# Kernel optimization log

Measured on AMD Instinct MI355X. Metric: run time of the kernel, lower is better.

## Reference

```python
import jax, jax.numpy as jnp
import numpy as np
from jax import lax

CROP = 4
DATA_RANGE = 255.0
KSIZE = 11


def _box_filter(x):
    # x: [B,1,H,W]; 11x11 uniform kernel, padding 5 (SAME), single channel
    k = jnp.ones((1, 1, KSIZE, KSIZE), dtype=x.dtype) / (KSIZE * KSIZE)
    return lax.conv_general_dilated(
        x, k, window_strides=(1, 1), padding=[(5, 5), (5, 5)],
        dimension_numbers=("NCHW", "OIHW", "NCHW"))


def setup_inputs() -> dict:
    key = jax.random.key(0)
    k1, k2 = jax.random.split(key)
    img1 = jax.random.uniform(k1, (16, 3, 512, 512), dtype=jnp.float32) * DATA_RANGE
    img2 = jax.random.uniform(k2, (16, 3, 512, 512), dtype=jnp.float32) * DATA_RANGE
    return {"img1": img1, "img2": img2}


def reference(img1, img2):
    # only_test_y_channel: take channel 0
    x1 = img1[:, 0:1, :, :]
    x2 = img2[:, 0:1, :, :]
    # crop_border = 4
    x1 = x1[:, :, CROP:-CROP, CROP:-CROP].astype(jnp.float32)
    x2 = x2[:, :, CROP:-CROP, CROP:-CROP].astype(jnp.float32)

    C1 = (0.01 * DATA_RANGE) ** 2
    C2 = (0.03 * DATA_RANGE) ** 2

    mu1 = _box_filter(x1)
    mu2 = _box_filter(x2)
    mu1_sq = mu1 * mu1
    mu2_sq = mu2 * mu2
    mu1_mu2 = mu1 * mu2
    sigma1_sq = _box_filter(x1 * x1) - mu1_sq
    sigma2_sq = _box_filter(x2 * x2) - mu2_sq
    sigma12 = _box_filter(x1 * x2) - mu1_mu2

    ssim_map = ((2 * mu1_mu2 + C1) * (2 * sigma12 + C2)) / (
        (mu1_sq + mu2_sq + C1) * (sigma1_sq + sigma2_sq + C2))
    return jnp.mean(ssim_map)
```

## Files before the change

### kernel.cpp

```cpp
#include <hip/hip_runtime.h>

#define CROPPX 4
#define H 504
#define W 504
#define IMG 512
#define NB 16
#define NCH 3
#define KS 11
#define RAD 5
#define TW 64
#define STRIP (TW + 2*RAD)
#define RPS 21
#define WPB 4
#define BROWS (RPS * WPB)
#define NYB 6
#define NXT 8
#define TOTAL (RPS + 2*RAD)

__global__ __launch_bounds__(256, 4) void ssim_main(const float* __restrict__ img1,
                                                    const float* __restrict__ img2,
                                                    float* __restrict__ partial) {
    const int lane = threadIdx.x & 63;
    const int wv   = threadIdx.x >> 6;
    const int gx0  = blockIdx.x * TW;
    const int y0   = blockIdx.y * BROWS + wv * RPS;
    const int b    = blockIdx.z;

    __shared__ float2 rowBuf[WPB][STRIP];
    float2* const myRow = rowBuf[wv];

    const float* p1 = img1 + (size_t)(b * NCH) * IMG * IMG + (size_t)CROPPX * IMG + CROPPX;
    const float* p2 = img2 + (size_t)(b * NCH) * IMG * IMG + (size_t)CROPPX * IMG + CROPPX;

    const int  c0   = gx0 - RAD + lane;
    const int  c0c  = min(max(c0, 0), W - 1);
    const bool c0ok = (unsigned)c0 < (unsigned)W;
    const int  c1   = c0 + 64;
    const int  c1c  = min(c1, W - 1);
    const bool c1ok = (unsigned)c1 < (unsigned)W;
    const bool lane2 = lane < (STRIP - 64);

    float r1[KS], r2[KS], r11[KS], r22[KS], r12[KS];
    #pragma unroll
    for (int j = 0; j < KS; ++j) { r1[j]=0.f; r2[j]=0.f; r11[j]=0.f; r22[j]=0.f; r12[j]=0.f; }

    float vs1 = 0.f, vs2 = 0.f, vs11 = 0.f, vs22 = 0.f, vs12 = 0.f;
    float ssum = 0.f;
    const float C1 = 6.5025f, C2 = 58.5225f;
    const float inv121 = 1.0f / 121.0f;
    const bool colValid = (gx0 + lane) < W;

    float a0, b0, a1 = 0.f, b1 = 0.f;
    {
        const int r  = y0 - RAD;
        const int rc = min(max(r, 0), H - 1);
        const bool rok = (unsigned)r < (unsigned)H;
        const size_t ro = (size_t)rc * IMG;
        const float ta0 = p1[ro + c0c], tb0 = p2[ro + c0c];
        a0 = (rok && c0ok) ? ta0 : 0.f;
        b0 = (rok && c0ok) ? tb0 : 0.f;
        if (lane2) {
            const float ta1 = p1[ro + c1c], tb1 = p2[ro + c1c];
            a1 = (rok && c1ok) ? ta1 : 0.f;
            b1 = (rok && c1ok) ? tb1 : 0.f;
        }
    }

    for (int base = 0; base < TOTAL; base += KS) {
        #pragma unroll
        for (int j = 0; j < KS; ++j) {
            const int iter = base + j;
            if (iter >= TOTAL) break;

            myRow[lane] = make_float2(a0, b0);
            if (lane2) myRow[64 + lane] = make_float2(a1, b1);

            if (iter + 1 < TOTAL) {
                const int r  = y0 - RAD + iter + 1;
                const int rc = min(max(r, 0), H - 1);
                const bool rok = (unsigned)r < (unsigned)H;
                const size_t ro = (size_t)rc * IMG;
                const float ta0 = p1[ro + c0c], tb0 = p2[ro + c0c];
                a0 = (rok && c0ok) ? ta0 : 0.f;
                b0 = (rok && c0ok) ? tb0 : 0.f;
                if (lane2) {
                    const float ta1 = p1[ro + c1c], tb1 = p2[ro + c1c];
                    a1 = (rok && c1ok) ? ta1 : 0.f;
                    b1 = (rok && c1ok) ? tb1 : 0.f;
                }
            }

            float h1 = 0.f, h2 = 0.f, h11 = 0.f, h22 = 0.f, h12 = 0.f;
            #pragma unroll
            for (int dx = 0; dx < KS; ++dx) {
                const float2 ab = myRow[lane + dx];
                h1 += ab.x;
                h2 += ab.y;
                h11 = fmaf(ab.x, ab.x, h11);
                h22 = fmaf(ab.y, ab.y, h22);
                h12 = fmaf(ab.x, ab.y, h12);
            }

            vs1  += h1  - r1[j];  r1[j]  = h1;
            vs2  += h2  - r2[j];  r2[j]  = h2;
            vs11 += h11 - r11[j]; r11[j] = h11;
            vs22 += h22 - r22[j]; r22[j] = h22;
            vs12 += h12 - r12[j]; r12[j] = h12;

            if (iter >= 2 * RAD && colValid) {
                const float mu1 = vs1 * inv121;
                const float mu2 = vs2 * inv121;
                const float mu1s = mu1 * mu1;
                const float mu2s = mu2 * mu2;
                const float m12  = mu1 * mu2;
                const float s1  = fmaf(vs11, inv121, -mu1s);
                const float s2  = fmaf(vs22, inv121, -mu2s);
                const float s12 = fmaf(vs12, inv121, -m12);
                const float num = (2.0f * m12 + C1) * (2.0f * s12 + C2);
                const float den = (mu1s + mu2s + C1) * (s1 + s2 + C2);
                ssum = fmaf(num, __builtin_amdgcn_rcpf(den), ssum);
            }
        }
    }

    for (int off = 32; off > 0; off >>= 1)
        ssum += __shfl_down(ssum, off);
    if (lane == 0) {
        const int bidx = (((blockIdx.z * gridDim.y + blockIdx.y) * gridDim.x + blockIdx.x) * WPB) + wv;
        partial[bidx] = ssum;
    }
}

__global__ __launch_bounds__(256) void ssim_final(const float* __restrict__ partial,
                                                  int n, float* __restrict__ out) {
    __shared__ double sh[256];
    double s = 0.0;
    for (int i = threadIdx.x; i < n; i += 256) s += (double)partial[i];
    sh[threadIdx.x] = s;
    __syncthreads();
    for (int stride = 128; stride > 0; stride >>= 1) {
        if (threadIdx.x < stride) sh[threadIdx.x] += sh[threadIdx.x + stride];
        __syncthreads();
    }
    if (threadIdx.x == 0)
        out[0] = (float)(sh[0] / ((double)NB * (double)H * (double)W));
}

extern "C" void kernel_launch(void* const* d_in, const int* in_sizes, int n_in,
                              void* d_out, int out_size, void* d_ws, size_t ws_size,
                              hipStream_t stream) {
    const float* img1 = (const float*)d_in[0];
    const float* img2 = (const float*)d_in[1];
    float* out = (float*)d_out;
    float* partial = (float*)d_ws;

    dim3 grid(NXT, NYB, NB);
    ssim_main<<<grid, 256, 0, stream>>>(img1, img2, partial);
    ssim_final<<<1, 256, 0, stream>>>(partial, NXT * NYB * NB * WPB, out);
}
```

Measured before the change: 145.1 us.

## Replace LDS row staging with per-thread direct global loads of the horizontal window

Removes the shared-memory row buffer. Each thread now loads its own 11-element horizontal window for both images straight from global memory, relying on cache for the overlap between neighbouring lanes. Column out-of-range values are zeroed with a precomputed mask only in edge blocks, and out-of-range rows are zeroed after the horizontal sum. This drops LDS writes and reads, but issues about eleven times more global load instructions per row and needs more registers, so the launch-bounds occupancy hint is lowered from 4 to 3.

```diff
diff --git a/kernel.cpp b/kernel.cpp
--- a/kernel.cpp
+++ b/kernel.cpp
@@ -9,7 +9,6 @@
 #define KS 11
 #define RAD 5
 #define TW 64
-#define STRIP (TW + 2*RAD)
 #define RPS 21
 #define WPB 4
 #define BROWS (RPS * WPB)
@@ -17,7 +16,7 @@
 #define NXT 8
 #define TOTAL (RPS + 2*RAD)
 
-__global__ __launch_bounds__(256, 4) void ssim_main(const float* __restrict__ img1,
+__global__ __launch_bounds__(256, 3) void ssim_main(const float* __restrict__ img1,
                                                     const float* __restrict__ img2,
                                                     float* __restrict__ partial) {
     const int lane = threadIdx.x & 63;
@@ -26,19 +25,18 @@
     const int y0   = blockIdx.y * BROWS + wv * RPS;
     const int b    = blockIdx.z;
 
-    __shared__ float2 rowBuf[WPB][STRIP];
-    float2* const myRow = rowBuf[wv];
-
     const float* p1 = img1 + (size_t)(b * NCH) * IMG * IMG + (size_t)CROPPX * IMG + CROPPX;
     const float* p2 = img2 + (size_t)(b * NCH) * IMG * IMG + (size_t)CROPPX * IMG + CROPPX;
 
-    const int  c0   = gx0 - RAD + lane;
-    const int  c0c  = min(max(c0, 0), W - 1);
-    const bool c0ok = (unsigned)c0 < (unsigned)W;
-    const int  c1   = c0 + 64;
-    const int  c1c  = min(c1, W - 1);
-    const bool c1ok = (unsigned)c1 < (unsigned)W;
-    const bool lane2 = lane < (STRIP - 64);
+    const int  c        = gx0 + lane;
+    const bool colValid = c < W;
+    const int  colBase  = c - RAD;
+    const bool boundary = (blockIdx.x == 0) || (blockIdx.x == NXT - 1);
+
+    float mk[KS];
+    #pragma unroll
+    for (int j = 0; j < KS; ++j)
+        mk[j] = ((unsigned)(colBase + j) < (unsigned)W) ? 1.f : 0.f;
 
     float r1[KS], r2[KS], r11[KS], r22[KS], r12[KS];
     #pragma unroll
@@ -48,22 +46,15 @@
     float ssum = 0.f;
     const float C1 = 6.5025f, C2 = 58.5225f;
     const float inv121 = 1.0f / 121.0f;
-    const bool colValid = (gx0 + lane) < W;
 
-    float a0, b0, a1 = 0.f, b1 = 0.f;
+    float na[KS], nb[KS];
     {
         const int r  = y0 - RAD;
         const int rc = min(max(r, 0), H - 1);
-        const bool rok = (unsigned)r < (unsigned)H;
-        const size_t ro = (size_t)rc * IMG;
-        const float ta0 = p1[ro + c0c], tb0 = p2[ro + c0c];
-        a0 = (rok && c0ok) ? ta0 : 0.f;
-        b0 = (rok && c0ok) ? tb0 : 0.f;
-        if (lane2) {
-            const float ta1 = p1[ro + c1c], tb1 = p2[ro + c1c];
-            a1 = (rok && c1ok) ? ta1 : 0.f;
-            b1 = (rok && c1ok) ? tb1 : 0.f;
-        }
+        const float* q1 = p1 + (size_t)rc * IMG + colBase;
+        const float* q2 = p2 + (size_t)rc * IMG + colBase;
+        #pragma unroll
+        for (int j = 0; j < KS; ++j) { na[j] = q1[j]; nb[j] = q2[j]; }
     }
 
     for (int base = 0; base < TOTAL; base += KS) {
@@ -72,34 +63,36 @@
             const int iter = base + j;
             if (iter >= TOTAL) break;
 
-            myRow[lane] = make_float2(a0, b0);
-            if (lane2) myRow[64 + lane] = make_float2(a1, b1);
+            float ca[KS], cb[KS];
+            #pragma unroll
+            for (int t = 0; t < KS; ++t) { ca[t] = na[t]; cb[t] = nb[t]; }
 
             if (iter + 1 < TOTAL) {
                 const int r  = y0 - RAD + iter + 1;
                 const int rc = min(max(r, 0), H - 1);
-                const bool rok = (unsigned)r < (unsigned)H;
-                const size_t ro = (size_t)rc * IMG;
-                const float ta0 = p1[ro + c0c], tb0 = p2[ro + c0c];
-                a0 = (rok && c0ok) ? ta0 : 0.f;
-                b0 = (rok && c0ok) ? tb0 : 0.f;
-                if (lane2) {
-                    const float ta1 = p1[ro + c1c], tb1 = p2[ro + c1c];
-                    a1 = (rok && c1ok) ? ta1 : 0.f;
-                    b1 = (rok && c1ok) ? tb1 : 0.f;
-                }
+                const float* q1 = p1 + (size_t)rc * IMG + colBase;
+                const float* q2 = p2 + (size_t)rc * IMG + colBase;
+                #pragma unroll
+                for (int t = 0; t < KS; ++t) { na[t] = q1[t]; nb[t] = q2[t]; }
+            }
+
+            if (boundary) {
+                #pragma unroll
+                for (int t = 0; t < KS; ++t) { ca[t] *= mk[t]; cb[t] *= mk[t]; }
             }
 
             float h1 = 0.f, h2 = 0.f, h11 = 0.f, h22 = 0.f, h12 = 0.f;
             #pragma unroll
-            for (int dx = 0; dx < KS; ++dx) {
-                const float2 ab = myRow[lane + dx];
-                h1 += ab.x;
-                h2 += ab.y;
-                h11 = fmaf(ab.x, ab.x, h11);
-                h22 = fmaf(ab.y, ab.y, h22);
-                h12 = fmaf(ab.x, ab.y, h12);
+            for (int t = 0; t < KS; ++t) {
+                h1 += ca[t];
+                h2 += cb[t];
+                h11 = fmaf(ca[t], ca[t], h11);
+                h22 = fmaf(cb[t], cb[t], h22);
+                h12 = fmaf(ca[t], cb[t], h12);
             }
+
+            const int rcur = y0 - RAD + iter;
+            if ((unsigned)rcur >= (unsigned)H) { h1 = 0.f; h2 = 0.f; h11 = 0.f; h22 = 0.f; h12 = 0.f; }
 
             vs1  += h1  - r1[j];  r1[j]  = h1;
             vs2  += h2  - r2[j];  r2[j]  = h2;
```

New measurement: 160.3 us. +10.5%, slower.
